# Kernel optimization log

Hardware: AMD Instinct MI355X
Metric: run time of the kernel (lower is better)

The kernel has to match this reference:

```python
import jax, jax.numpy as jnp
import numpy as np

D = 42            # node hidden dim
ED = 10           # edge feature dim
B = 512           # graphs per batch
NU, EU = 16384, 32768   # solute nodes/edges (32 nodes per graph)
NV, EV = 20480, 40960   # solvent nodes/edges (40 nodes per graph)
STEPS = 6


def setup_inputs() -> dict:
    key = jax.random.key(0)
    ks = iter(jax.random.split(key, 48))
    nrm = lambda shape, s: jax.random.normal(next(ks), shape, dtype=jnp.float32) * s
    inp = {}
    inp["su_x"] = nrm((NU, D), 1.0)
    inp["su_e"] = nrm((EU, ED), 1.0)
    inp["su_src"] = jax.random.randint(next(ks), (EU,), 0, NU, dtype=jnp.int32)
    inp["su_dst"] = jax.random.randint(next(ks), (EU,), 0, NU, dtype=jnp.int32)
    inp["sv_x"] = nrm((NV, D), 1.0)
    inp["sv_e"] = nrm((EV, ED), 1.0)
    inp["sv_src"] = jax.random.randint(next(ks), (EV,), 0, NV, dtype=jnp.int32)
    inp["sv_dst"] = jax.random.randint(next(ks), (EV,), 0, NV, dtype=jnp.int32)
    for p in ("su", "sv"):
        inp[p + "_lin0_w"] = nrm((D, D), D ** -0.5)
        inp[p + "_lin0_b"] = jnp.zeros((D,), jnp.float32)
        inp[p + "_msg_w"] = nrm((D, D), D ** -0.5)
        inp[p + "_msg_b"] = jnp.zeros((D,), jnp.float32)
        inp[p + "_en1_w"] = nrm((ED, ED), ED ** -0.5)
        inp[p + "_en1_b"] = jnp.zeros((ED,), jnp.float32)
        inp[p + "_en2_w"] = nrm((ED, D * D), 0.02)  # small scale keeps 6-step recursion stable
        inp[p + "_en2_b"] = jnp.zeros((D * D,), jnp.float32)
        inp[p + "_conv_b"] = jnp.zeros((D,), jnp.float32)
    inp["fc1_w"] = nrm((4 * D, 256), (4 * D) ** -0.5)
    inp["fc1_b"] = jnp.zeros((256,), jnp.float32)
    inp["fc2_w"] = nrm((256, 128), 256 ** -0.5)
    inp["fc2_b"] = jnp.zeros((128,), jnp.float32)
    inp["fc3_w"] = nrm((128, 1), 128 ** -0.5)
    inp["fc3_b"] = jnp.zeros((1,), jnp.float32)
    return inp


def _gather(x, efeat, src, dst, lw, lb, mw, mb, e1w, e1b, e2w, e2b, cb, n_nodes):
    """GatherModel: lin0 + 6 x (NNConv(sum, residual=identity, bias) -> relu -> message_layer -> relu) + skip."""
    init = x
    out = jax.nn.relu(x @ lw + lb)
    # Edge network depends only on static edge features -> compute per-edge 42x42 once.
    We = (jax.nn.relu(efeat @ e1w + e1b) @ e2w + e2b).reshape(-1, D, D)  # [E, D, D]
    for _ in range(STEPS):
        msg = jnp.einsum('ei,eio->eo', out[src], We)                    # gather + per-edge matvec
        agg = jax.ops.segment_sum(msg, dst, num_segments=n_nodes)      # scatter-add
        m = jax.nn.relu(agg + out + cb)                                 # residual (identity) + bias, then relu
        out = jax.nn.relu(m @ mw + mb)
    return out + init


def reference(su_x, su_e, su_src, su_dst, sv_x, sv_e, sv_src, sv_dst,
              su_lin0_w, su_lin0_b, su_msg_w, su_msg_b, su_en1_w, su_en1_b, su_en2_w, su_en2_b, su_conv_b,
              sv_lin0_w, sv_lin0_b, sv_msg_w, sv_msg_b, sv_en1_w, sv_en1_b, sv_en2_w, sv_en2_b, sv_conv_b,
              fc1_w, fc1_b, fc2_w, fc2_b, fc3_w, fc3_b):
    su = _gather(su_x, su_e, su_src, su_dst, su_lin0_w, su_lin0_b, su_msg_w, su_msg_b,
                 su_en1_w, su_en1_b, su_en2_w, su_en2_b, su_conv_b, NU)
    sv = _gather(sv_x, sv_e, sv_src, sv_dst, sv_lin0_w, sv_lin0_b, sv_msg_w, sv_msg_b,
                 sv_en1_w, sv_en1_b, sv_en2_w, sv_en2_b, sv_conv_b, NV)
    # per-graph mean pooling (equal-sized graphs -> reshape)
    su_emb = su.reshape(B, NU // B, D).mean(axis=1)          # [B, D]
    sv_emb = sv.reshape(B, NV // B, D).mean(axis=1)
    su_fin = jnp.concatenate([su_emb, su_emb], axis=1)       # [B, 2D]
    sv_fin = jnp.concatenate([sv_emb, sv_emb], axis=1)
    su_g = su_fin.mean(axis=0, keepdims=True)                # [1, 2D] (code means over batch)
    sv_g = sv_fin.mean(axis=0, keepdims=True)
    comb = jnp.concatenate([su_g, sv_g], axis=1)             # [1, 4D]
    h = jax.nn.relu(comb @ fc1_w + fc1_b)                    # dropout is identity at inference
    h = jax.nn.relu(h @ fc2_w + fc2_b)
    pred = h @ fc3_w + fc3_b                                 # [1, 1]
    interaction = jnp.zeros((su.shape[0], sv.shape[0]), jnp.float32)
    return pred, interaction
```

## Files before the change

### kernel.cpp

```cpp
#include <hip/hip_runtime.h>

#define D   42
#define ED  10
#define NU  16384
#define EU  32768
#define NV  20480
#define EV  40960
#define NT  (NU + NV)
#define ET  (EU + EV)
#define GJ  462
#define GP  464
#define STEPS 6

typedef float floatx4 __attribute__((ext_vector_type(4)));

__global__ __launch_bounds__(256) void k_zero(floatx4* __restrict__ p, long n4,
                                              float* __restrict__ tail, int ntail) {
    long stride = (long)gridDim.x * 256;
    floatx4 z = (floatx4)(0.f);
    for (long i = blockIdx.x * 256L + threadIdx.x; i < n4; i += stride)
        p[i] = z;
    if (blockIdx.x == 0 && threadIdx.x < ntail)
        tail[threadIdx.x] = 0.f;
}

__global__ void k_prep(const float* __restrict__ su_w2, const float* __restrict__ su_b2,
                       const float* __restrict__ sv_w2, const float* __restrict__ sv_b2,
                       float* __restrict__ A, float* __restrict__ mean) {
    int gid = blockIdx.x * 256 + threadIdx.x;
    if (gid < 128) mean[gid] = 0.f;
    if (gid >= 2 * D * GP) return;
    int phase = gid / (D * GP);
    int r = gid - phase * D * GP;
    int i = r / GP, j = r - i * GP;
    const float* w2 = phase ? sv_w2 : su_w2;
    const float* b2 = phase ? sv_b2 : su_b2;
    float v = 0.f;
    if (j < GJ) {
        int k = j / D, o = j - k * D;
        v = (k < ED) ? w2[k * (D * D) + i * D + o] : b2[i * D + o];
    }
    A[gid] = v;
}

__global__ void k_lin0(const float* __restrict__ su_x, const float* __restrict__ sv_x,
                       const float* __restrict__ su_w, const float* __restrict__ su_b,
                       const float* __restrict__ sv_w, const float* __restrict__ sv_b,
                       float* __restrict__ out) {
    int gid = blockIdx.x * 256 + threadIdx.x;
    if (gid >= NT * D) return;
    int n = gid / D, o = gid - n * D;
    const float *x, *w, *b; int nl;
    if (n < NU) { x = su_x; w = su_w; b = su_b; nl = n; }
    else        { x = sv_x; w = sv_w; b = sv_b; nl = n - NU; }
    float s = b[o];
    #pragma unroll
    for (int i = 0; i < D; i++) s += x[nl * D + i] * w[i * D + o];
    out[gid] = fmaxf(s, 0.f);
}

__global__ void k_zcnt(int* __restrict__ p, int n) {
    int gid = blockIdx.x * 256 + threadIdx.x;
    if (gid < n) p[gid] = 0;
}

__global__ void k_count(const int* __restrict__ su_src, const int* __restrict__ su_dst,
                        const int* __restrict__ sv_src, const int* __restrict__ sv_dst,
                        int* __restrict__ outDeg, int* __restrict__ inDeg) {
    int e = blockIdx.x * 256 + threadIdx.x;
    if (e >= ET) return;
    int src, dst;
    if (e < EU) { src = su_src[e];           dst = su_dst[e]; }
    else        { src = sv_src[e - EU] + NU; dst = sv_dst[e - EU] + NU; }
    atomicAdd(&outDeg[src], 1);
    atomicAdd(&inDeg[dst], 1);
}

__global__ __launch_bounds__(1024) void k_scan(const int* __restrict__ degO, int* __restrict__ offO,
                                               const int* __restrict__ degI, int* __restrict__ offI) {
    __shared__ int part[1024];
    int t = threadIdx.x;
    for (int a = 0; a < 2; a++) {
        const int* deg = a ? degI : degO;
        int* off = a ? offI : offO;
        int loc[36];
        int base = t * 36;
        int s = 0;
        #pragma unroll
        for (int j = 0; j < 36; j++) { loc[j] = s; s += deg[base + j]; }
        part[t] = s;
        __syncthreads();
        for (int d = 1; d < 1024; d <<= 1) {
            int v = (t >= d) ? part[t - d] : 0;
            __syncthreads();
            part[t] += v;
            __syncthreads();
        }
        int excl = part[t] - s;
        #pragma unroll
        for (int j = 0; j < 36; j++) off[base + j] = excl + loc[j];
        if (t == 1023) off[NT] = excl + s;
        __syncthreads();
    }
}

__global__ void k_place(const int* __restrict__ su_src, const int* __restrict__ su_dst,
                        const int* __restrict__ sv_src, const int* __restrict__ sv_dst,
                        const int* __restrict__ offO, int* __restrict__ cntO,
                        const int* __restrict__ offI, int* __restrict__ cntI,
                        int* __restrict__ inList, int* __restrict__ srcSorted,
                        int* __restrict__ pOf) {
    int e = blockIdx.x * 256 + threadIdx.x;
    if (e >= ET) return;
    int src, dst;
    if (e < EU) { src = su_src[e];           dst = su_dst[e]; }
    else        { src = sv_src[e - EU] + NU; dst = sv_dst[e - EU] + NU; }
    int p = offO[src] + atomicAdd(&cntO[src], 1);
    int q = offI[dst] + atomicAdd(&cntI[dst], 1);
    inList[q] = p;
    srcSorted[p] = src;
    pOf[e] = p;
}

__global__ void k_edgeh(const float* __restrict__ su_e, const float* __restrict__ sv_e,
                        const float* __restrict__ su_w1, const float* __restrict__ su_b1,
                        const float* __restrict__ sv_w1, const float* __restrict__ sv_b1,
                        const int* __restrict__ pOf, float* __restrict__ hs) {
    __shared__ float w1s[2][ED * ED];
    __shared__ float b1s[2][ED];
    int tid = threadIdx.x;
    if (tid < ED * ED) { w1s[0][tid] = su_w1[tid]; w1s[1][tid] = sv_w1[tid]; }
    if (tid < ED)      { b1s[0][tid] = su_b1[tid]; b1s[1][tid] = sv_b1[tid]; }
    __syncthreads();
    int e = blockIdx.x * 256 + tid;
    if (e >= ET) return;
    int ph = (e >= EU);
    const float* ef = ph ? (sv_e + (size_t)(e - EU) * ED) : (su_e + (size_t)e * ED);
    float v[ED];
    #pragma unroll
    for (int j = 0; j < ED; j++) v[j] = ef[j];
    size_t p = (size_t)pOf[e] * 12;
    #pragma unroll
    for (int k = 0; k < ED; k++) {
        float s = b1s[ph][k];
        #pragma unroll
        for (int j = 0; j < ED; j++) s += v[j] * w1s[ph][j * ED + k];
        hs[p + k] = fmaxf(s, 0.f);
    }
    hs[p + 10] = 1.f;
    hs[p + 11] = 0.f;
}

__global__ __launch_bounds__(512, 1) void k_gmsg(const float* __restrict__ out,
                                                 const float* __restrict__ A,
                                                 const int* __restrict__ offO,
                                                 const int* __restrict__ srcSorted,
                                                 const float* __restrict__ hs,
                                                 float* __restrict__ msg) {
    __shared__ float A_lds[D * GP];
    __shared__ float g_lds[32 * GP];
    __shared__ float out_lds[32 * 44];
    int tid = threadIdx.x;
    int n0 = blockIdx.x * 32;
    const floatx4* Ag = (const floatx4*)(A + (n0 >= NU ? D * GP : 0));
    floatx4* Al4 = (floatx4*)A_lds;
    for (int idx = tid; idx < D * GP / 4; idx += 512) Al4[idx] = Ag[idx];
    for (int idx = tid; idx < 32 * D; idx += 512) {
        int nn = idx / D, i = idx - nn * D;
        out_lds[nn * 44 + i] = out[(size_t)(n0 + nn) * D + i];
    }
    __syncthreads();

    int tj = tid & 127;
    int tn = tid >> 7;
    if (tj < 116) {
        floatx4 acc[8];
        #pragma unroll
        for (int r = 0; r < 8; r++) acc[r] = (floatx4)(0.f);
        for (int i = 0; i < D; i++) {
            floatx4 a = Al4[i * 116 + tj];
            #pragma unroll
            for (int r = 0; r < 8; r++) acc[r] += a * out_lds[(tn * 8 + r) * 44 + i];
        }
        floatx4* gl4 = (floatx4*)g_lds;
        #pragma unroll
        for (int r = 0; r < 8; r++) gl4[(tn * 8 + r) * 116 + tj] = acc[r];
    }
    __syncthreads();

    int p0 = offO[n0], p1 = offO[n0 + 32];
    int nwork = (p1 - p0) * D;
    for (int idx = tid; idx < nwork; idx += 512) {
        int pr = idx / D, o = idx - pr * D;
        int p = p0 + pr;
        int local = srcSorted[p] - n0;
        const float* hrow = hs + (size_t)p * 12;
        const float* grow = g_lds + local * GP;
        float s = 0.f;
        #pragma unroll
        for (int k = 0; k <= ED; k++) s += hrow[k] * grow[k * D + o];
        msg[(size_t)p * D + o] = s;
    }
}

__global__ __launch_bounds__(256) void k_upd(const int* __restrict__ offI,
                                             const int* __restrict__ inList,
                                             const float* __restrict__ msg,
                                             float* __restrict__ out,
                                             const float* __restrict__ su_mw, const float* __restrict__ su_mb,
                                             const float* __restrict__ su_cb,
                                             const float* __restrict__ sv_mw, const float* __restrict__ sv_mb,
                                             const float* __restrict__ sv_cb) {
    __shared__ float mw_lds[D * D];
    __shared__ float m_lds[32 * 44];
    int tid = threadIdx.x;
    int n0 = blockIdx.x * 32;
    int ph = (n0 >= NU);
    const float* mw = ph ? sv_mw : su_mw;
    const float* mb = ph ? sv_mb : su_mb;
    const float* cb = ph ? sv_cb : su_cb;
    for (int idx = tid; idx < D * D; idx += 256) mw_lds[idx] = mw[idx];
    for (int idx = tid; idx < 32 * D; idx += 256) {
        int nn = idx / D, o = idx - nn * D;
        int n = n0 + nn;
        int q0 = offI[n], q1 = offI[n + 1];
        float s = out[(size_t)n * D + o] + cb[o];
        for (int q = q0; q < q1; q++) s += msg[(size_t)inList[q] * D + o];
        m_lds[nn * 44 + o] = fmaxf(s, 0.f);
    }
    __syncthreads();
    for (int idx = tid; idx < 32 * D; idx += 256) {
        int nn = idx / D, o = idx - nn * D;
        float s = mb[o];
        #pragma unroll
        for (int i = 0; i < D; i++) s += m_lds[nn * 44 + i] * mw_lds[i * D + o];
        out[(size_t)(n0 + nn) * D + o] = fmaxf(s, 0.f);
    }
}

__global__ void k_reduce(const float* __restrict__ out, const float* __restrict__ su_x,
                         const float* __restrict__ sv_x, float* __restrict__ mean) {
    __shared__ float sdata[6 * D];
    int tid = threadIdx.x;
    int bid = blockIdx.x;
    int n0, ph, nl0;
    const float* x;
    if (bid < NU / 128) { ph = 0; n0 = bid * 128;                 nl0 = n0;      x = su_x; }
    else                { ph = 1; n0 = NU + (bid - NU/128) * 128; nl0 = n0 - NU; x = sv_x; }
    if (tid < 6 * D) {
        int o = tid % D, r = tid / D;
        float acc = 0.f;
        for (int nn = r; nn < 128; nn += 6)
            acc += out[(size_t)(n0 + nn) * D + o] + x[(size_t)(nl0 + nn) * D + o];
        sdata[r * D + o] = acc;
    }
    __syncthreads();
    if (tid < D) {
        float tot = 0.f;
        #pragma unroll
        for (int r = 0; r < 6; r++) tot += sdata[r * D + tid];
        atomicAdd(&mean[ph * D + tid], tot);
    }
}

__global__ void k_mlp(const float* __restrict__ mean,
                      const float* __restrict__ fc1w, const float* __restrict__ fc1b,
                      const float* __restrict__ fc2w, const float* __restrict__ fc2b,
                      const float* __restrict__ fc3w, const float* __restrict__ fc3b,
                      float* __restrict__ outp) {
    __shared__ float c[4 * D];
    __shared__ float h1[256];
    __shared__ float h2[128];
    int t = threadIdx.x;
    if (t < 4 * D) {
        float v;
        if (t < 2 * D) v = mean[t < D ? t : t - D] * (1.f / NU);
        else { int q = t - 2 * D; v = mean[D + (q < D ? q : q - D)] * (1.f / NV); }
        c[t] = v;
    }
    __syncthreads();
    float s = fc1b[t];
    for (int j = 0; j < 4 * D; j++) s += c[j] * fc1w[j * 256 + t];
    h1[t] = fmaxf(s, 0.f);
    __syncthreads();
    if (t < 128) {
        float s2 = fc2b[t];
        for (int j = 0; j < 256; j++) s2 += h1[j] * fc2w[j * 128 + t];
        h2[t] = fmaxf(s2, 0.f);
    }
    __syncthreads();
    if (t == 0) {
        float s3 = fc3b[0];
        for (int j = 0; j < 128; j++) s3 += h2[j] * fc3w[j];
        outp[0] = s3;
    }
}

extern "C" void kernel_launch(void* const* d_in, const int* in_sizes, int n_in,
                              void* d_out, int out_size, void* d_ws, size_t ws_size,
                              hipStream_t stream) {
    const float* su_x     = (const float*)d_in[0];
    const float* su_e     = (const float*)d_in[1];
    const int*   su_src   = (const int*)d_in[2];
    const int*   su_dst   = (const int*)d_in[3];
    const float* sv_x     = (const float*)d_in[4];
    const float* sv_e     = (const float*)d_in[5];
    const int*   sv_src   = (const int*)d_in[6];
    const int*   sv_dst   = (const int*)d_in[7];
    const float* su_lin0w = (const float*)d_in[8];
    const float* su_lin0b = (const float*)d_in[9];
    const float* su_msgw  = (const float*)d_in[10];
    const float* su_msgb  = (const float*)d_in[11];
    const float* su_en1w  = (const float*)d_in[12];
    const float* su_en1b  = (const float*)d_in[13];
    const float* su_en2w  = (const float*)d_in[14];
    const float* su_en2b  = (const float*)d_in[15];
    const float* su_convb = (const float*)d_in[16];
    const float* sv_lin0w = (const float*)d_in[17];
    const float* sv_lin0b = (const float*)d_in[18];
    const float* sv_msgw  = (const float*)d_in[19];
    const float* sv_msgb  = (const float*)d_in[20];
    const float* sv_en1w  = (const float*)d_in[21];
    const float* sv_en1b  = (const float*)d_in[22];
    const float* sv_en2w  = (const float*)d_in[23];
    const float* sv_en2b  = (const float*)d_in[24];
    const float* sv_convb = (const float*)d_in[25];
    const float* fc1w     = (const float*)d_in[26];
    const float* fc1b     = (const float*)d_in[27];
    const float* fc2w     = (const float*)d_in[28];
    const float* fc2b     = (const float*)d_in[29];
    const float* fc3w     = (const float*)d_in[30];
    const float* fc3b     = (const float*)d_in[31];

    float* ws   = (float*)d_ws;
    float* out  = ws;
    float* msg  = out  + (size_t)NT * D;
    float* hs   = msg  + (size_t)ET * D;
    float* A    = hs   + (size_t)ET * 12;
    float* mean = A    + (size_t)2 * D * GP;
    int* ib     = (int*)(mean + 128);
    int* outDeg = ib;
    int* inDeg  = outDeg + NT;
    int* outCnt = inDeg  + NT;
    int* inCnt  = outCnt + NT;
    int* outOff = inCnt  + NT;
    int* inOff  = outOff + (NT + 1);
    int* inList = inOff  + (NT + 1);
    int* srcS   = inList + ET;
    int* pOf    = srcS   + ET;

    {
        long n4 = ((long)out_size * 4) / 16;
        int ntail = (int)(out_size - n4 * 4);
        float* tailp = (float*)d_out + n4 * 4;
        k_zero<<<2048, 256, 0, stream>>>((floatx4*)d_out, n4, tailp, ntail);
    }

    k_prep<<<(2 * D * GP + 255) / 256, 256, 0, stream>>>(su_en2w, su_en2b, sv_en2w, sv_en2b, A, mean);
    k_lin0<<<(NT * D + 255) / 256, 256, 0, stream>>>(su_x, sv_x, su_lin0w, su_lin0b, sv_lin0w, sv_lin0b, out);

    k_zcnt<<<(4 * NT + 255) / 256, 256, 0, stream>>>(outDeg, 4 * NT);
    k_count<<<(ET + 255) / 256, 256, 0, stream>>>(su_src, su_dst, sv_src, sv_dst, outDeg, inDeg);
    k_scan<<<1, 1024, 0, stream>>>(outDeg, outOff, inDeg, inOff);
    k_place<<<(ET + 255) / 256, 256, 0, stream>>>(su_src, su_dst, sv_src, sv_dst,
                                                  outOff, outCnt, inOff, inCnt, inList, srcS, pOf);
    k_edgeh<<<(ET + 255) / 256, 256, 0, stream>>>(su_e, sv_e, su_en1w, su_en1b, sv_en1w, sv_en1b, pOf, hs);

    for (int s = 0; s < STEPS; s++) {
        k_gmsg<<<NT / 32, 512, 0, stream>>>(out, A, outOff, srcS, hs, msg);
        k_upd<<<NT / 32, 256, 0, stream>>>(inOff, inList, msg, out,
                                           su_msgw, su_msgb, su_convb, sv_msgw, sv_msgb, sv_convb);
    }

    k_reduce<<<NU / 128 + NV / 128, 256, 0, stream>>>(out, su_x, sv_x, mean);
    k_mlp<<<1, 256, 0, stream>>>(mean, fc1w, fc1b, fc2w, fc2b, fc3w, fc3b, (float*)d_out);
}
```

Measured before the change: 872.5 us.

## Retile message and update GEMMs with transposed LDS tiles and direct A reads

The message kernel stops staging the per-phase A matrix in LDS and reads it straight from global/L2. The node tile is stored transposed so each thread computes a 4x8 register block, and the smaller LDS footprint allows two blocks per CU. The update kernel gets a register-blocked 4x4 GEMM over a transposed message tile and a padded weight tile, launched with 128 threads. The output zeroing kernel is replaced by hipMemsetAsync. The risk is that global A reads in the inner loop cost more than the LDS reads they replace, and that the update kernel leaves many threads idle.

New measurement: 1.077 ms. +23.4%, slower.

```diff
diff --git a/kernel.cpp b/kernel.cpp
--- a/kernel.cpp
+++ b/kernel.cpp
@@ -13,16 +13,6 @@
 #define STEPS 6
 
 typedef float floatx4 __attribute__((ext_vector_type(4)));
-
-__global__ __launch_bounds__(256) void k_zero(floatx4* __restrict__ p, long n4,
-                                              float* __restrict__ tail, int ntail) {
-    long stride = (long)gridDim.x * 256;
-    floatx4 z = (floatx4)(0.f);
-    for (long i = blockIdx.x * 256L + threadIdx.x; i < n4; i += stride)
-        p[i] = z;
-    if (blockIdx.x == 0 && threadIdx.x < ntail)
-        tail[threadIdx.x] = 0.f;
-}
 
 __global__ void k_prep(const float* __restrict__ su_w2, const float* __restrict__ su_b2,
                        const float* __restrict__ sv_w2, const float* __restrict__ sv_b2,
@@ -151,40 +141,46 @@
     hs[p + 11] = 0.f;
 }
 
-__global__ __launch_bounds__(512, 1) void k_gmsg(const float* __restrict__ out,
-                                                 const float* __restrict__ A,
-                                                 const int* __restrict__ offO,
-                                                 const int* __restrict__ srcSorted,
-                                                 const float* __restrict__ hs,
-                                                 float* __restrict__ msg) {
-    __shared__ float A_lds[D * GP];
+__global__ __launch_bounds__(512, 2) void k_gmsg2(const float* __restrict__ out,
+                                                  const float* __restrict__ A,
+                                                  const int* __restrict__ offO,
+                                                  const int* __restrict__ srcSorted,
+                                                  const float* __restrict__ hs,
+                                                  float* __restrict__ msg) {
+    __shared__ float outT[D * 36];
     __shared__ float g_lds[32 * GP];
-    __shared__ float out_lds[32 * 44];
     int tid = threadIdx.x;
     int n0 = blockIdx.x * 32;
-    const floatx4* Ag = (const floatx4*)(A + (n0 >= NU ? D * GP : 0));
-    floatx4* Al4 = (floatx4*)A_lds;
-    for (int idx = tid; idx < D * GP / 4; idx += 512) Al4[idx] = Ag[idx];
+    const floatx4* A4 = (const floatx4*)(A + (n0 >= NU ? D * GP : 0));
+
     for (int idx = tid; idx < 32 * D; idx += 512) {
-        int nn = idx / D, i = idx - nn * D;
-        out_lds[nn * 44 + i] = out[(size_t)(n0 + nn) * D + i];
-    }
-    __syncthreads();
-
-    int tj = tid & 127;
-    int tn = tid >> 7;
-    if (tj < 116) {
-        floatx4 acc[8];
-        #pragma unroll
-        for (int r = 0; r < 8; r++) acc[r] = (floatx4)(0.f);
-        for (int i = 0; i < D; i++) {
-            floatx4 a = Al4[i * 116 + tj];
+        int nn = idx & 31, i = idx >> 5;
+        outT[i * 36 + nn] = out[(size_t)(n0 + nn) * D + i];
+    }
+    __syncthreads();
+
+    if (tid < 464) {
+        int cg = tid % 58, rg = tid / 58;
+        const floatx4* oT4 = (const floatx4*)outT;
+        floatx4 acc[4][2];
+        #pragma unroll
+        for (int r = 0; r < 4; r++) { acc[r][0] = (floatx4)(0.f); acc[r][1] = (floatx4)(0.f); }
+        for (int k = 0; k < D; k++) {
+            floatx4 a0 = A4[k * 116 + 2 * cg];
+            floatx4 a1 = A4[k * 116 + 2 * cg + 1];
+            floatx4 o4 = oT4[k * 9 + rg];
             #pragma unroll
-            for (int r = 0; r < 8; r++) acc[r] += a * out_lds[(tn * 8 + r) * 44 + i];
+            for (int r = 0; r < 4; r++) {
+                acc[r][0] += a0 * o4[r];
+                acc[r][1] += a1 * o4[r];
+            }
         }
         floatx4* gl4 = (floatx4*)g_lds;
         #pragma unroll
-        for (int r = 0; r < 8; r++) gl4[(tn * 8 + r) * 116 + tj] = acc[r];
+        for (int r = 0; r < 4; r++) {
+            gl4[(4 * rg + r) * 116 + 2 * cg]     = acc[r][0];
+            gl4[(4 * rg + r) * 116 + 2 * cg + 1] = acc[r][1];
+        }
     }
     __syncthreads();
 
@@ -203,38 +199,57 @@
     }
 }
 
-__global__ __launch_bounds__(256) void k_upd(const int* __restrict__ offI,
-                                             const int* __restrict__ inList,
-                                             const float* __restrict__ msg,
-                                             float* __restrict__ out,
-                                             const float* __restrict__ su_mw, const float* __restrict__ su_mb,
-                                             const float* __restrict__ su_cb,
-                                             const float* __restrict__ sv_mw, const float* __restrict__ sv_mb,
-                                             const float* __restrict__ sv_cb) {
-    __shared__ float mw_lds[D * D];
-    __shared__ float m_lds[32 * 44];
+__global__ __launch_bounds__(128) void k_upd2(const int* __restrict__ offI,
+                                              const int* __restrict__ inList,
+                                              const float* __restrict__ msg,
+                                              float* __restrict__ out,
+                                              const float* __restrict__ su_mw, const float* __restrict__ su_mb,
+                                              const float* __restrict__ su_cb,
+                                              const float* __restrict__ sv_mw, const float* __restrict__ sv_mb,
+                                              const float* __restrict__ sv_cb) {
+    __shared__ float mT[D * 36];
+    __shared__ float mw_lds[D * 48];
     int tid = threadIdx.x;
     int n0 = blockIdx.x * 32;
     int ph = (n0 >= NU);
     const float* mw = ph ? sv_mw : su_mw;
     const float* mb = ph ? sv_mb : su_mb;
     const float* cb = ph ? sv_cb : su_cb;
-    for (int idx = tid; idx < D * D; idx += 256) mw_lds[idx] = mw[idx];
-    for (int idx = tid; idx < 32 * D; idx += 256) {
-        int nn = idx / D, o = idx - nn * D;
+    for (int idx = tid; idx < D * 48; idx += 128) {
+        int i = idx / 48, o = idx - i * 48;
+        mw_lds[idx] = (o < D) ? mw[i * D + o] : 0.f;
+    }
+    for (int idx = tid; idx < 32 * D; idx += 128) {
+        int nn = idx & 31, o = idx >> 5;
         int n = n0 + nn;
         int q0 = offI[n], q1 = offI[n + 1];
         float s = out[(size_t)n * D + o] + cb[o];
         for (int q = q0; q < q1; q++) s += msg[(size_t)inList[q] * D + o];
-        m_lds[nn * 44 + o] = fmaxf(s, 0.f);
-    }
-    __syncthreads();
-    for (int idx = tid; idx < 32 * D; idx += 256) {
-        int nn = idx / D, o = idx - nn * D;
-        float s = mb[o];
-        #pragma unroll
-        for (int i = 0; i < D; i++) s += m_lds[nn * 44 + i] * mw_lds[i * D + o];
-        out[(size_t)(n0 + nn) * D + o] = fmaxf(s, 0.f);
+        mT[o * 36 + nn] = fmaxf(s, 0.f);
+    }
+    __syncthreads();
+    if (tid < 88) {
+        int cg = tid % 11, rg = tid / 11;
+        const floatx4* mT4 = (const floatx4*)mT;
+        const floatx4* mw4 = (const floatx4*)mw_lds;
+        floatx4 acc[4];
+        #pragma unroll
+        for (int r = 0; r < 4; r++) acc[r] = (floatx4)(0.f);
+        for (int k = 0; k < D; k++) {
+            floatx4 a = mT4[k * 9 + rg];
+            floatx4 w = mw4[k * 12 + cg];
+            #pragma unroll
+            for (int r = 0; r < 4; r++) acc[r] += w * a[r];
+        }
+        #pragma unroll
+        for (int r = 0; r < 4; r++) {
+            size_t row = (size_t)(n0 + 4 * rg + r) * D;
+            #pragma unroll
+            for (int c = 0; c < 4; c++) {
+                int col = 4 * cg + c;
+                if (col < D) out[row + col] = fmaxf(acc[r][c] + mb[col], 0.f);
+            }
+        }
     }
 }
 
@@ -349,12 +364,7 @@
     int* srcS   = inList + ET;
     int* pOf    = srcS   + ET;
 
-    {
-        long n4 = ((long)out_size * 4) / 16;
-        int ntail = (int)(out_size - n4 * 4);
-        float* tailp = (float*)d_out + n4 * 4;
-        k_zero<<<2048, 256, 0, stream>>>((floatx4*)d_out, n4, tailp, ntail);
-    }
+    hipMemsetAsync(d_out, 0, (size_t)out_size * sizeof(float), stream);
 
     k_prep<<<(2 * D * GP + 255) / 256, 256, 0, stream>>>(su_en2w, su_en2b, sv_en2w, sv_en2b, A, mean);
     k_lin0<<<(NT * D + 255) / 256, 256, 0, stream>>>(su_x, sv_x, su_lin0w, su_lin0b, sv_lin0w, sv_lin0b, out);
@@ -367,9 +377,9 @@
     k_edgeh<<<(ET + 255) / 256, 256, 0, stream>>>(su_e, sv_e, su_en1w, su_en1b, sv_en1w, sv_en1b, pOf, hs);
 
     for (int s = 0; s < STEPS; s++) {
-        k_gmsg<<<NT / 32, 512, 0, stream>>>(out, A, outOff, srcS, hs, msg);
-        k_upd<<<NT / 32, 256, 0, stream>>>(inOff, inList, msg, out,
-                                           su_msgw, su_msgb, su_convb, sv_msgw, sv_msgb, sv_convb);
+        k_gmsg2<<<NT / 32, 512, 0, stream>>>(out, A, outOff, srcS, hs, msg);
+        k_upd2<<<NT / 32, 128, 0, stream>>>(inOff, inList, msg, out,
+                                            su_msgw, su_msgb, su_convb, sv_msgw, sv_msgb, sv_convb);
     }
 
     k_reduce<<<NU / 128 + NV / 128, 256, 0, stream>>>(out, su_x, sv_x, mean);
```

## Fuse node update into the message kernel with double-buffered messages

Applied to the files above, without the earlier changes.

Each step's node update (message aggregation, relu, msg linear) now runs at the head of the next step's message kernel. Step 0 performs lin0 inside the same kernel, so the separate lin0 launch goes away, and a final update kernel finishes the last step. Messages are double-buffered so reads of the previous step do not collide with writes of the current one, and the output zeroing now uses hipMemsetAsync. The goal is fewer launches and less global round-tripping of the node state. In exchange, the fused kernel uses more LDS and registers, and the GEMM thread mapping is reworked to read transposed node tiles.

After: 846.9 us. 2.9% less time.

```diff
diff --git a/kernel.cpp b/kernel.cpp
--- a/kernel.cpp
+++ b/kernel.cpp
@@ -13,16 +13,6 @@
 #define STEPS 6
 
 typedef float floatx4 __attribute__((ext_vector_type(4)));
-
-__global__ __launch_bounds__(256) void k_zero(floatx4* __restrict__ p, long n4,
-                                              float* __restrict__ tail, int ntail) {
-    long stride = (long)gridDim.x * 256;
-    floatx4 z = (floatx4)(0.f);
-    for (long i = blockIdx.x * 256L + threadIdx.x; i < n4; i += stride)
-        p[i] = z;
-    if (blockIdx.x == 0 && threadIdx.x < ntail)
-        tail[threadIdx.x] = 0.f;
-}
 
 __global__ void k_prep(const float* __restrict__ su_w2, const float* __restrict__ su_b2,
                        const float* __restrict__ sv_w2, const float* __restrict__ sv_b2,
@@ -41,22 +31,6 @@
         v = (k < ED) ? w2[k * (D * D) + i * D + o] : b2[i * D + o];
     }
     A[gid] = v;
-}
-
-__global__ void k_lin0(const float* __restrict__ su_x, const float* __restrict__ sv_x,
-                       const float* __restrict__ su_w, const float* __restrict__ su_b,
-                       const float* __restrict__ sv_w, const float* __restrict__ sv_b,
-                       float* __restrict__ out) {
-    int gid = blockIdx.x * 256 + threadIdx.x;
-    if (gid >= NT * D) return;
-    int n = gid / D, o = gid - n * D;
-    const float *x, *w, *b; int nl;
-    if (n < NU) { x = su_x; w = su_w; b = su_b; nl = n; }
-    else        { x = sv_x; w = sv_w; b = sv_b; nl = n - NU; }
-    float s = b[o];
-    #pragma unroll
-    for (int i = 0; i < D; i++) s += x[nl * D + i] * w[i * D + o];
-    out[gid] = fmaxf(s, 0.f);
 }
 
 __global__ void k_zcnt(int* __restrict__ p, int n) {
@@ -151,40 +125,96 @@
     hs[p + 11] = 0.f;
 }
 
-__global__ __launch_bounds__(512, 1) void k_gmsg(const float* __restrict__ out,
+__global__ __launch_bounds__(512, 1) void k_step(float* __restrict__ out,
                                                  const float* __restrict__ A,
                                                  const int* __restrict__ offO,
                                                  const int* __restrict__ srcSorted,
                                                  const float* __restrict__ hs,
-                                                 float* __restrict__ msg) {
+                                                 float* __restrict__ msgW,
+                                                 const float* __restrict__ msgR,
+                                                 const int* __restrict__ offI,
+                                                 const int* __restrict__ inList,
+                                                 const float* __restrict__ su_x,
+                                                 const float* __restrict__ sv_x,
+                                                 const float* __restrict__ su_W, const float* __restrict__ su_b,
+                                                 const float* __restrict__ sv_W, const float* __restrict__ sv_b,
+                                                 const float* __restrict__ su_cb, const float* __restrict__ sv_cb,
+                                                 int first) {
     __shared__ float A_lds[D * GP];
     __shared__ float g_lds[32 * GP];
-    __shared__ float out_lds[32 * 44];
+    __shared__ float outT[D * 36];
+    __shared__ float mT[D * 36];
+    __shared__ float w_lds[D * 48];
     int tid = threadIdx.x;
     int n0 = blockIdx.x * 32;
-    const floatx4* Ag = (const floatx4*)(A + (n0 >= NU ? D * GP : 0));
+    int ph = (n0 >= NU);
+
+    const floatx4* Ag = (const floatx4*)(A + (ph ? D * GP : 0));
     floatx4* Al4 = (floatx4*)A_lds;
     for (int idx = tid; idx < D * GP / 4; idx += 512) Al4[idx] = Ag[idx];
+
+    const float* W = ph ? sv_W : su_W;
+    const float* b = ph ? sv_b : su_b;
+    for (int idx = tid; idx < D * 48; idx += 512) {
+        int i = idx / 48, o = idx - i * 48;
+        w_lds[idx] = (o < D) ? W[i * D + o] : 0.f;
+    }
+
+    if (first) {
+        const float* x = ph ? (sv_x + (size_t)(n0 - NU) * D) : (su_x + (size_t)n0 * D);
+        for (int idx = tid; idx < 32 * D; idx += 512) {
+            int i = idx % D, nn = idx / D;
+            mT[i * 36 + nn] = x[(size_t)nn * D + i];
+        }
+    } else {
+        const float* cb = ph ? sv_cb : su_cb;
+        for (int idx = tid; idx < 32 * D; idx += 512) {
+            int o = idx % D, nn = idx / D;
+            int n = n0 + nn;
+            int q0 = offI[n], q1 = offI[n + 1];
+            float s = out[(size_t)n * D + o] + cb[o];
+            for (int q = q0; q < q1; q++) s += msgR[(size_t)inList[q] * D + o];
+            mT[o * 36 + nn] = fmaxf(s, 0.f);
+        }
+    }
+    __syncthreads();
+
     for (int idx = tid; idx < 32 * D; idx += 512) {
-        int nn = idx / D, i = idx - nn * D;
-        out_lds[nn * 44 + i] = out[(size_t)(n0 + nn) * D + i];
-    }
-    __syncthreads();
-
-    int tj = tid & 127;
-    int tn = tid >> 7;
-    if (tj < 116) {
-        floatx4 acc[8];
-        #pragma unroll
-        for (int r = 0; r < 8; r++) acc[r] = (floatx4)(0.f);
-        for (int i = 0; i < D; i++) {
-            floatx4 a = Al4[i * 116 + tj];
+        int o = idx % D, nn = idx / D;
+        float s = b[o];
+        #pragma unroll
+        for (int i = 0; i < D; i++) s += mT[i * 36 + nn] * w_lds[i * 48 + o];
+        float v = fmaxf(s, 0.f);
+        out[(size_t)(n0 + nn) * D + o] = v;
+        outT[o * 36 + nn] = v;
+    }
+    __syncthreads();
+
+    if (tid < 232) {
+        int cg = tid % 58, ng = tid / 58;
+        const floatx4* oT4 = (const floatx4*)outT;
+        floatx4 acc[8][2];
+        #pragma unroll
+        for (int r = 0; r < 8; r++) { acc[r][0] = (floatx4)(0.f); acc[r][1] = (floatx4)(0.f); }
+        for (int k = 0; k < D; k++) {
+            floatx4 a0 = Al4[k * 116 + 2 * cg];
+            floatx4 a1 = Al4[k * 116 + 2 * cg + 1];
+            floatx4 o0 = oT4[k * 9 + 2 * ng];
+            floatx4 o1 = oT4[k * 9 + 2 * ng + 1];
             #pragma unroll
-            for (int r = 0; r < 8; r++) acc[r] += a * out_lds[(tn * 8 + r) * 44 + i];
+            for (int r = 0; r < 4; r++) {
+                acc[r][0]     += a0 * o0[r];
+                acc[r][1]     += a1 * o0[r];
+                acc[r + 4][0] += a0 * o1[r];
+                acc[r + 4][1] += a1 * o1[r];
+            }
         }
         floatx4* gl4 = (floatx4*)g_lds;
         #pragma unroll
-        for (int r = 0; r < 8; r++) gl4[(tn * 8 + r) * 116 + tj] = acc[r];
+        for (int r = 0; r < 8; r++) {
+            gl4[(8 * ng + r) * 116 + 2 * cg]     = acc[r][0];
+            gl4[(8 * ng + r) * 116 + 2 * cg + 1] = acc[r][1];
+        }
     }
     __syncthreads();
 
@@ -199,20 +229,20 @@
         float s = 0.f;
         #pragma unroll
         for (int k = 0; k <= ED; k++) s += hrow[k] * grow[k * D + o];
-        msg[(size_t)p * D + o] = s;
-    }
-}
-
-__global__ __launch_bounds__(256) void k_upd(const int* __restrict__ offI,
-                                             const int* __restrict__ inList,
-                                             const float* __restrict__ msg,
-                                             float* __restrict__ out,
-                                             const float* __restrict__ su_mw, const float* __restrict__ su_mb,
-                                             const float* __restrict__ su_cb,
-                                             const float* __restrict__ sv_mw, const float* __restrict__ sv_mb,
-                                             const float* __restrict__ sv_cb) {
+        msgW[(size_t)p * D + o] = s;
+    }
+}
+
+__global__ __launch_bounds__(256) void k_updF(const int* __restrict__ offI,
+                                              const int* __restrict__ inList,
+                                              const float* __restrict__ msg,
+                                              float* __restrict__ out,
+                                              const float* __restrict__ su_mw, const float* __restrict__ su_mb,
+                                              const float* __restrict__ su_cb,
+                                              const float* __restrict__ sv_mw, const float* __restrict__ sv_mb,
+                                              const float* __restrict__ sv_cb) {
     __shared__ float mw_lds[D * D];
-    __shared__ float m_lds[32 * 44];
+    __shared__ float mloc[32 * 44];
     int tid = threadIdx.x;
     int n0 = blockIdx.x * 32;
     int ph = (n0 >= NU);
@@ -221,19 +251,19 @@
     const float* cb = ph ? sv_cb : su_cb;
     for (int idx = tid; idx < D * D; idx += 256) mw_lds[idx] = mw[idx];
     for (int idx = tid; idx < 32 * D; idx += 256) {
-        int nn = idx / D, o = idx - nn * D;
+        int o = idx % D, nn = idx / D;
         int n = n0 + nn;
         int q0 = offI[n], q1 = offI[n + 1];
         float s = out[(size_t)n * D + o] + cb[o];
         for (int q = q0; q < q1; q++) s += msg[(size_t)inList[q] * D + o];
-        m_lds[nn * 44 + o] = fmaxf(s, 0.f);
+        mloc[nn * 44 + o] = fmaxf(s, 0.f);
     }
     __syncthreads();
     for (int idx = tid; idx < 32 * D; idx += 256) {
-        int nn = idx / D, o = idx - nn * D;
+        int o = idx % D, nn = idx / D;
         float s = mb[o];
         #pragma unroll
-        for (int i = 0; i < D; i++) s += m_lds[nn * 44 + i] * mw_lds[i * D + o];
+        for (int i = 0; i < D; i++) s += mloc[nn * 44 + i] * mw_lds[i * D + o];
         out[(size_t)(n0 + nn) * D + o] = fmaxf(s, 0.f);
     }
 }
@@ -334,8 +364,9 @@
 
     float* ws   = (float*)d_ws;
     float* out  = ws;
-    float* msg  = out  + (size_t)NT * D;
-    float* hs   = msg  + (size_t)ET * D;
+    float* msg0 = out  + (size_t)NT * D;
+    float* msg1 = msg0 + (size_t)ET * D;
+    float* hs   = msg1 + (size_t)ET * D;
     float* A    = hs   + (size_t)ET * 12;
     float* mean = A    + (size_t)2 * D * GP;
     int* ib     = (int*)(mean + 128);
@@ -349,15 +380,9 @@
     int* srcS   = inList + ET;
     int* pOf    = srcS   + ET;
 
-    {
-        long n4 = ((long)out_size * 4) / 16;
-        int ntail = (int)(out_size - n4 * 4);
-        float* tailp = (float*)d_out + n4 * 4;
-        k_zero<<<2048, 256, 0, stream>>>((floatx4*)d_out, n4, tailp, ntail);
-    }
+    hipMemsetAsync(d_out, 0, (size_t)out_size * sizeof(float), stream);
 
     k_prep<<<(2 * D * GP + 255) / 256, 256, 0, stream>>>(su_en2w, su_en2b, sv_en2w, sv_en2b, A, mean);
-    k_lin0<<<(NT * D + 255) / 256, 256, 0, stream>>>(su_x, sv_x, su_lin0w, su_lin0b, sv_lin0w, sv_lin0b, out);
 
     k_zcnt<<<(4 * NT + 255) / 256, 256, 0, stream>>>(outDeg, 4 * NT);
     k_count<<<(ET + 255) / 256, 256, 0, stream>>>(su_src, su_dst, sv_src, sv_dst, outDeg, inDeg);
@@ -366,11 +391,24 @@
                                                   outOff, outCnt, inOff, inCnt, inList, srcS, pOf);
     k_edgeh<<<(ET + 255) / 256, 256, 0, stream>>>(su_e, sv_e, su_en1w, su_en1b, sv_en1w, sv_en1b, pOf, hs);
 
+    float* mbuf[2] = { msg0, msg1 };
     for (int s = 0; s < STEPS; s++) {
-        k_gmsg<<<NT / 32, 512, 0, stream>>>(out, A, outOff, srcS, hs, msg);
-        k_upd<<<NT / 32, 256, 0, stream>>>(inOff, inList, msg, out,
-                                           su_msgw, su_msgb, su_convb, sv_msgw, sv_msgb, sv_convb);
-    }
+        float* mw_ = mbuf[s & 1];
+        float* mr_ = mbuf[(s & 1) ^ 1];
+        if (s == 0) {
+            k_step<<<NT / 32, 512, 0, stream>>>(out, A, outOff, srcS, hs, mw_, nullptr,
+                                                inOff, inList, su_x, sv_x,
+                                                su_lin0w, su_lin0b, sv_lin0w, sv_lin0b,
+                                                su_convb, sv_convb, 1);
+        } else {
+            k_step<<<NT / 32, 512, 0, stream>>>(out, A, outOff, srcS, hs, mw_, mr_,
+                                                inOff, inList, su_x, sv_x,
+                                                su_msgw, su_msgb, sv_msgw, sv_msgb,
+                                                su_convb, sv_convb, 0);
+        }
+    }
+    k_updF<<<NT / 32, 256, 0, stream>>>(inOff, inList, mbuf[(STEPS - 1) & 1], out,
+                                        su_msgw, su_msgb, su_convb, sv_msgw, sv_msgb, sv_convb);
 
     k_reduce<<<NU / 128 + NV / 128, 256, 0, stream>>>(out, su_x, sv_x, mean);
     k_mlp<<<1, 256, 0, stream>>>(mean, fc1w, fc1b, fc2w, fc2b, fc3w, fc3b, (float*)d_out);
```
